# Kernel tuning notes

Measured on AMD Instinct MI355X. Metric: run time of the kernel, lower is better.

## Reference

```python
import jax, jax.numpy as jnp
import numpy as np

NEG_INF = -1e9  # matches the torch module's masked_fill value of -1000000000.0


def setup_inputs() -> dict:
    key = jax.random.key(0)
    kq, kk, kv, km = jax.random.split(key, 4)
    b, h, L, d = 2, 16, 2048, 64
    q = jax.random.normal(kq, (b, h, L, d), dtype=jnp.float32)
    k = jax.random.normal(kk, (b, h, L, d), dtype=jnp.float32)
    v = jax.random.normal(kv, (b, h, L, d), dtype=jnp.float32)
    attn_mask = jax.random.randint(km, (b, 1, L, L), 0, 2, dtype=jnp.int32)
    return {"q": q, "k": k, "v": v, "attn_mask": attn_mask}


def reference(q, k, v, attn_mask):
    # att = q @ k^T / sqrt(d)   -> [b, h, Lq, Lk]
    scale = 1.0 / jnp.sqrt(jnp.asarray(q.shape[-1], q.dtype))
    att = jnp.einsum("bhqd,bhkd->bhqk", q, k) * scale
    # masked positions (mask == 0) filled with -1e9 before softmax
    att = jnp.where(attn_mask == 0, jnp.asarray(NEG_INF, att.dtype), att)
    att = jax.nn.softmax(att, axis=-1)
    # x = att @ v -> [b, h, Lq, d]
    return jnp.einsum("bhqk,bhkd->bhqd", att, v)
```

## Files before the change

kernel.cpp:

```cpp
#include <hip/hip_runtime.h>


typedef unsigned int u32;
typedef unsigned short u16;
typedef unsigned long long u64;

#define BH 32
#define Lseq 2048
#define Dh 64
#define BM 64

typedef __attribute__((ext_vector_type(8))) short frag_ab;
typedef __attribute__((ext_vector_type(4))) float frag_cd;

__device__ __forceinline__ u16 f2bf(float f) {
    u32 u = __float_as_uint(f);
    u32 r = u + 0x7FFFu + ((u >> 16) & 1u);
    return (u16)(r >> 16);
}

__global__ __launch_bounds__(256) void prep(
    const float* __restrict__ k, const float* __restrict__ v,
    const int* __restrict__ mask,
    u16* __restrict__ kb, u16* __restrict__ vtb, u64* __restrict__ bm)
{
    const int blk = blockIdx.x, tid = threadIdx.x;
    if (blk < 512) {
        int t0 = blk * 256 + tid;
        #pragma unroll
        for (int i = 0; i < 8; i++) {
            int idx = t0 + i * 131072;
            float4 f = ((const float4*)k)[idx];
            ushort4 r;
            r.x = f2bf(f.x); r.y = f2bf(f.y); r.z = f2bf(f.z); r.w = f2bf(f.w);
            ((ushort4*)kb)[idx] = r;
        }
    } else if (blk < 1024) {
        __shared__ u16 T[64 * 72];
        for (int j = 0; j < 2; j++) {
            int job = (blk - 512) * 2 + j;
            int bh = job >> 5, kt = job & 31;
            __syncthreads();
            #pragma unroll
            for (int i = 0; i < 4; i++) {
                int idx = tid + 256 * i;
                int key = idx >> 4, ds = idx & 15;
                float4 f = *(const float4*)(v + ((size_t)(bh * Lseq + kt * 64 + key)) * Dh + ds * 4);
                int d0 = ds * 4;
                T[(d0 + 0) * 72 + key] = f2bf(f.x);
                T[(d0 + 1) * 72 + key] = f2bf(f.y);
                T[(d0 + 2) * 72 + key] = f2bf(f.z);
                T[(d0 + 3) * 72 + key] = f2bf(f.w);
            }
            __syncthreads();
            #pragma unroll
            for (int i = 0; i < 4; i++) {
                int idx = tid + 256 * i;
                int d = idx >> 4, ks = idx & 15;
                *(uint2*)(vtb + ((size_t)(bh * Dh + d)) * Lseq + kt * 64 + ks * 4) =
                    *(const uint2*)&T[d * 72 + ks * 4];
            }
        }
    } else {
        int wv = (blk - 1024) * 4 + (tid >> 6);
        int lane = tid & 63;
        for (int i = 0; i < 64; i++) {
            int widx = wv * 64 + i;
            int rowp = widx >> 5, kt = widx & 31;
            int val = mask[(size_t)rowp * Lseq + kt * 64 + lane];
            u64 bal = __ballot(val != 0);
            if (lane == 0) bm[(size_t)kt * 4096 + rowp] = bal;
        }
    }
}

__global__ __launch_bounds__(256, 4)
void attn_mfma(const float* __restrict__ qg, const u16* __restrict__ kb,
               const u16* __restrict__ vtb, const u64* __restrict__ bm,
               float* __restrict__ outg)
{
    const int bh = blockIdx.y, b = bh >> 4;
    const int q0 = blockIdx.x * BM;
    const int tid = threadIdx.x;
    const int wave = tid >> 6, lane = tid & 63;
    const int c = lane & 15, quad = lane >> 4;
    const int row = q0 + 16 * wave + c;

    __shared__ u16 Ks[64 * 72];
    __shared__ u16 Vs[64 * 72];
    __shared__ u16 Ps[4][16 * 72];

    frag_ab qf[2];
    #pragma unroll
    for (int ks = 0; ks < 2; ks++) {
        const float* p = qg + ((size_t)bh * Lseq + row) * Dh + 32 * ks + 8 * quad;
        float4 f0 = *(const float4*)p;
        float4 f1 = *(const float4*)(p + 4);
        union { u32 w[4]; frag_ab f; } uq;
        uq.w[0] = (u32)f2bf(f0.x * 0.125f) | ((u32)f2bf(f0.y * 0.125f) << 16);
        uq.w[1] = (u32)f2bf(f0.z * 0.125f) | ((u32)f2bf(f0.w * 0.125f) << 16);
        uq.w[2] = (u32)f2bf(f1.x * 0.125f) | ((u32)f2bf(f1.y * 0.125f) << 16);
        uq.w[3] = (u32)f2bf(f1.z * 0.125f) | ((u32)f2bf(f1.w * 0.125f) << 16);
        qf[ks] = uq.f;
    }

    frag_cd o_acc[4];
    #pragma unroll
    for (int dt = 0; dt < 4; dt++) o_acc[dt] = (frag_cd){0.f, 0.f, 0.f, 0.f};
    float m_run = -1e30f, l_run = 0.f;

    for (int kt = 0; kt < Lseq / 64; ++kt) {
        __syncthreads();
        {
            const uint4* ksrc = (const uint4*)(kb + ((size_t)bh * Lseq + kt * 64) * Dh);
            #pragma unroll
            for (int i = 0; i < 2; i++) {
                int idx = tid + 256 * i;
                int key = idx >> 3, ds = idx & 7;
                *(uint4*)&Ks[key * 72 + ds * 8] = ksrc[idx];
            }
            #pragma unroll
            for (int i = 0; i < 2; i++) {
                int idx = tid + 256 * i;
                int d = idx >> 3, k8 = idx & 7;
                *(uint4*)&Vs[d * 72 + k8 * 8] =
                    *(const uint4*)(vtb + ((size_t)bh * Dh + d) * Lseq + kt * 64 + k8 * 8);
            }
        }
        const u64 mw = bm[(size_t)kt * 4096 + b * 2048 + row];
        __syncthreads();

        frag_cd s_acc[4];
        #pragma unroll
        for (int t = 0; t < 4; t++) s_acc[t] = (frag_cd){0.f, 0.f, 0.f, 0.f};
        #pragma unroll
        for (int t = 0; t < 4; t++) {
            frag_ab kf0 = *(const frag_ab*)&Ks[(16 * t + c) * 72 + 8 * quad];
            frag_ab kf1 = *(const frag_ab*)&Ks[(16 * t + c) * 72 + 32 + 8 * quad];
            s_acc[t] = __builtin_amdgcn_mfma_f32_16x16x32_bf16(kf0, qf[0], s_acc[t], 0, 0, 0);
            s_acc[t] = __builtin_amdgcn_mfma_f32_16x16x32_bf16(kf1, qf[1], s_acc[t], 0, 0, 0);
        }

        float mx = s_acc[0][0];
        #pragma unroll
        for (int t = 0; t < 4; t++)
            #pragma unroll
            for (int r = 0; r < 4; r++) mx = fmaxf(mx, s_acc[t][r]);
        mx = fmaxf(mx, __shfl_xor(mx, 16));
        mx = fmaxf(mx, __shfl_xor(mx, 32));
        const float mnew = fmaxf(m_run, mx);
        const float alpha = __expf(m_run - mnew);
        m_run = mnew;

        float lsum = 0.f;
        #pragma unroll
        for (int t = 0; t < 4; t++) {
            u32 mbits = (u32)(mw >> (16 * t + 4 * quad)) & 0xFu;
            #pragma unroll
            for (int r = 0; r < 4; r++) {
                float pv = __expf(s_acc[t][r] - mnew);
                pv = ((mbits >> r) & 1u) ? pv : 0.f;
                s_acc[t][r] = pv;
                lsum += pv;
            }
        }
        l_run = l_run * alpha + lsum;
        #pragma unroll
        for (int dt = 0; dt < 4; dt++) o_acc[dt] *= alpha;

        #pragma unroll
        for (int t = 0; t < 4; t++) {
            u32 p0 = __builtin_amdgcn_perm(__float_as_uint(s_acc[t][1]),
                                           __float_as_uint(s_acc[t][0]), 0x07060302u);
            u32 p1 = __builtin_amdgcn_perm(__float_as_uint(s_acc[t][3]),
                                           __float_as_uint(s_acc[t][2]), 0x07060302u);
            *(uint2*)&Ps[wave][c * 72 + 16 * t + 4 * quad] = make_uint2(p0, p1);
        }
        frag_ab pf0 = *(const frag_ab*)&Ps[wave][c * 72 + 8 * quad];
        frag_ab pf1 = *(const frag_ab*)&Ps[wave][c * 72 + 32 + 8 * quad];

        #pragma unroll
        for (int dt = 0; dt < 4; dt++) {
            frag_ab vf0 = *(const frag_ab*)&Vs[(16 * dt + c) * 72 + 8 * quad];
            frag_ab vf1 = *(const frag_ab*)&Vs[(16 * dt + c) * 72 + 32 + 8 * quad];
            o_acc[dt] = __builtin_amdgcn_mfma_f32_16x16x32_bf16(vf0, pf0, o_acc[dt], 0, 0, 0);
            o_acc[dt] = __builtin_amdgcn_mfma_f32_16x16x32_bf16(vf1, pf1, o_acc[dt], 0, 0, 0);
        }
    }

    float l = l_run;
    l += __shfl_xor(l, 16);
    l += __shfl_xor(l, 32);
    const float inv = 1.0f / l;
    float* orow = outg + ((size_t)bh * Lseq + row) * Dh;
    #pragma unroll
    for (int dt = 0; dt < 4; dt++) {
        *(float4*)(orow + 16 * dt + 4 * quad) =
            make_float4(o_acc[dt][0] * inv, o_acc[dt][1] * inv,
                        o_acc[dt][2] * inv, o_acc[dt][3] * inv);
    }
}

extern "C" void kernel_launch(void* const* d_in, const int* in_sizes, int n_in,
                              void* d_out, int out_size, void* d_ws, size_t ws_size,
                              hipStream_t stream) {
    const float* q    = (const float*)d_in[0];
    const float* k    = (const float*)d_in[1];
    const float* v    = (const float*)d_in[2];
    const int*   mask = (const int*)d_in[3];
    float* out = (float*)d_out;

    char* ws = (char*)d_ws;
    u16* kb  = (u16*)(ws);
    u16* vtb = (u16*)(ws + 8388608);
    u64* bmp = (u64*)(ws + 16777216);

    hipLaunchKernelGGL(prep, dim3(1536), dim3(256), 0, stream, k, v, mask, kb, vtb, bmp);
    hipLaunchKernelGGL(attn_mfma, dim3(Lseq / BM, BH), dim3(256), 0, stream,
                       q, kb, vtb, bmp, out);
}
```

Before: 208.9 us.

## Double-buffer K/V tiles, process two query groups per wave, use exp2 with folded scale

The attention kernel now handles 128 query rows per block, two 16-row groups per wave, so each K/V fragment read from shared memory feeds twice as many MFMAs. K/V tiles are double-buffered, with the next tile prefetched into registers during compute. The softmax scale times log2(e) is folded into the bf16 K conversion so exp2f can replace __expf. The O rescale is skipped when no row max changes, and the prep kernel is split into finer-grained blocks. Higher register use lowers occupancy, and there are half as many blocks.

```diff
diff --git a/kernel.cpp b/kernel.cpp
--- a/kernel.cpp
+++ b/kernel.cpp
@@ -8,7 +8,7 @@
 #define BH 32
 #define Lseq 2048
 #define Dh 64
-#define BM 64
+#define QK_SCALE 0.180336879f
 
 typedef __attribute__((ext_vector_type(8))) short frag_ab;
 typedef __attribute__((ext_vector_type(4))) float frag_cd;
@@ -25,47 +25,45 @@
     u16* __restrict__ kb, u16* __restrict__ vtb, u64* __restrict__ bm)
 {
     const int blk = blockIdx.x, tid = threadIdx.x;
-    if (blk < 512) {
-        int t0 = blk * 256 + tid;
-        #pragma unroll
-        for (int i = 0; i < 8; i++) {
-            int idx = t0 + i * 131072;
+    if (blk < 1024) {
+        #pragma unroll
+        for (int i = 0; i < 4; i++) {
+            int idx = blk * 1024 + i * 256 + tid;
             float4 f = ((const float4*)k)[idx];
             ushort4 r;
-            r.x = f2bf(f.x); r.y = f2bf(f.y); r.z = f2bf(f.z); r.w = f2bf(f.w);
+            r.x = f2bf(f.x * QK_SCALE); r.y = f2bf(f.y * QK_SCALE);
+            r.z = f2bf(f.z * QK_SCALE); r.w = f2bf(f.w * QK_SCALE);
             ((ushort4*)kb)[idx] = r;
         }
-    } else if (blk < 1024) {
+    } else if (blk < 2048) {
         __shared__ u16 T[64 * 72];
-        for (int j = 0; j < 2; j++) {
-            int job = (blk - 512) * 2 + j;
-            int bh = job >> 5, kt = job & 31;
-            __syncthreads();
-            #pragma unroll
-            for (int i = 0; i < 4; i++) {
-                int idx = tid + 256 * i;
-                int key = idx >> 4, ds = idx & 15;
-                float4 f = *(const float4*)(v + ((size_t)(bh * Lseq + kt * 64 + key)) * Dh + ds * 4);
-                int d0 = ds * 4;
-                T[(d0 + 0) * 72 + key] = f2bf(f.x);
-                T[(d0 + 1) * 72 + key] = f2bf(f.y);
-                T[(d0 + 2) * 72 + key] = f2bf(f.z);
-                T[(d0 + 3) * 72 + key] = f2bf(f.w);
-            }
-            __syncthreads();
-            #pragma unroll
-            for (int i = 0; i < 4; i++) {
-                int idx = tid + 256 * i;
-                int d = idx >> 4, ks = idx & 15;
-                *(uint2*)(vtb + ((size_t)(bh * Dh + d)) * Lseq + kt * 64 + ks * 4) =
-                    *(const uint2*)&T[d * 72 + ks * 4];
-            }
+        int job = blk - 1024;
+        int bh = job >> 5, kt = job & 31;
+        #pragma unroll
+        for (int i = 0; i < 4; i++) {
+            int idx = tid + 256 * i;
+            int key = idx >> 4, ds = idx & 15;
+            float4 f = *(const float4*)(v + ((size_t)(bh * Lseq + kt * 64 + key)) * Dh + ds * 4);
+            int d0 = ds * 4;
+            T[(d0 + 0) * 72 + key] = f2bf(f.x);
+            T[(d0 + 1) * 72 + key] = f2bf(f.y);
+            T[(d0 + 2) * 72 + key] = f2bf(f.z);
+            T[(d0 + 3) * 72 + key] = f2bf(f.w);
+        }
+        __syncthreads();
+        #pragma unroll
+        for (int i = 0; i < 4; i++) {
+            int idx = tid + 256 * i;
+            int d = idx >> 4, ks = idx & 15;
+            *(uint2*)(vtb + ((size_t)(bh * Dh + d)) * Lseq + kt * 64 + ks * 4) =
+                *(const uint2*)&T[d * 72 + ks * 4];
         }
     } else {
-        int wv = (blk - 1024) * 4 + (tid >> 6);
+        int wv = (blk - 2048) * 4 + (tid >> 6);
         int lane = tid & 63;
-        for (int i = 0; i < 64; i++) {
-            int widx = wv * 64 + i;
+        #pragma unroll
+        for (int i = 0; i < 16; i++) {
+            int widx = wv * 16 + i;
             int rowp = widx >> 5, kt = widx & 31;
             int val = mask[(size_t)rowp * Lseq + kt * 64 + lane];
             u64 bal = __ballot(val != 0);
@@ -74,130 +72,176 @@
     }
 }
 
-__global__ __launch_bounds__(256, 4)
+__global__ __launch_bounds__(256, 2)
 void attn_mfma(const float* __restrict__ qg, const u16* __restrict__ kb,
                const u16* __restrict__ vtb, const u64* __restrict__ bm,
                float* __restrict__ outg)
 {
     const int bh = blockIdx.y, b = bh >> 4;
-    const int q0 = blockIdx.x * BM;
+    const int q0 = blockIdx.x * 128;
     const int tid = threadIdx.x;
     const int wave = tid >> 6, lane = tid & 63;
     const int c = lane & 15, quad = lane >> 4;
-    const int row = q0 + 16 * wave + c;
-
-    __shared__ u16 Ks[64 * 72];
-    __shared__ u16 Vs[64 * 72];
-    __shared__ u16 Ps[4][16 * 72];
-
-    frag_ab qf[2];
+
+    __shared__ u16 Ks[2][64 * 72];
+    __shared__ u16 Vs[2][64 * 72];
+    __shared__ u16 Ps[4][2][16 * 72];
+
+    frag_ab qf[2][2];
     #pragma unroll
-    for (int ks = 0; ks < 2; ks++) {
-        const float* p = qg + ((size_t)bh * Lseq + row) * Dh + 32 * ks + 8 * quad;
-        float4 f0 = *(const float4*)p;
-        float4 f1 = *(const float4*)(p + 4);
-        union { u32 w[4]; frag_ab f; } uq;
-        uq.w[0] = (u32)f2bf(f0.x * 0.125f) | ((u32)f2bf(f0.y * 0.125f) << 16);
-        uq.w[1] = (u32)f2bf(f0.z * 0.125f) | ((u32)f2bf(f0.w * 0.125f) << 16);
-        uq.w[2] = (u32)f2bf(f1.x * 0.125f) | ((u32)f2bf(f1.y * 0.125f) << 16);
-        uq.w[3] = (u32)f2bf(f1.z * 0.125f) | ((u32)f2bf(f1.w * 0.125f) << 16);
-        qf[ks] = uq.f;
-    }
-
-    frag_cd o_acc[4];
+    for (int g = 0; g < 2; g++)
+        #pragma unroll
+        for (int ks = 0; ks < 2; ks++) {
+            const float* p = qg + ((size_t)bh * Lseq + q0 + 32 * wave + 16 * g + c) * Dh
+                                + 32 * ks + 8 * quad;
+            float4 f0 = *(const float4*)p;
+            float4 f1 = *(const float4*)(p + 4);
+            union { u32 w[4]; frag_ab f; } uq;
+            uq.w[0] = (u32)f2bf(f0.x) | ((u32)f2bf(f0.y) << 16);
+            uq.w[1] = (u32)f2bf(f0.z) | ((u32)f2bf(f0.w) << 16);
+            uq.w[2] = (u32)f2bf(f1.x) | ((u32)f2bf(f1.y) << 16);
+            uq.w[3] = (u32)f2bf(f1.z) | ((u32)f2bf(f1.w) << 16);
+            qf[g][ks] = uq.f;
+        }
+
+    frag_cd o_acc[4][2];
     #pragma unroll
-    for (int dt = 0; dt < 4; dt++) o_acc[dt] = (frag_cd){0.f, 0.f, 0.f, 0.f};
-    float m_run = -1e30f, l_run = 0.f;
-
-    for (int kt = 0; kt < Lseq / 64; ++kt) {
-        __syncthreads();
-        {
-            const uint4* ksrc = (const uint4*)(kb + ((size_t)bh * Lseq + kt * 64) * Dh);
+    for (int dt = 0; dt < 4; dt++)
+        #pragma unroll
+        for (int g = 0; g < 2; g++) o_acc[dt][g] = (frag_cd){0.f, 0.f, 0.f, 0.f};
+    float m_run[2] = {-1e30f, -1e30f};
+    float l_run[2] = {0.f, 0.f};
+
+    {
+        const uint4* ksrc = (const uint4*)(kb + ((size_t)bh * Lseq) * Dh);
+        #pragma unroll
+        for (int i = 0; i < 2; i++) {
+            int idx = tid + 256 * i;
+            *(uint4*)&Ks[0][(idx >> 3) * 72 + (idx & 7) * 8] = ksrc[idx];
+            *(uint4*)&Vs[0][(idx >> 3) * 72 + (idx & 7) * 8] =
+                *(const uint4*)(vtb + ((size_t)(bh * Dh + (idx >> 3))) * Lseq + (idx & 7) * 8);
+        }
+    }
+    __syncthreads();
+
+    for (int kt = 0; kt < 32; ++kt) {
+        const int cur = kt & 1, nxt = cur ^ 1;
+        const bool has_next = (kt + 1) < 32;
+
+        u64 mw[2];
+        #pragma unroll
+        for (int g = 0; g < 2; g++)
+            mw[g] = bm[(size_t)kt * 4096 + b * 2048 + q0 + 32 * wave + 16 * g + c];
+
+        uint4 kr[2], vr[2];
+        if (has_next) {
+            const uint4* ksrc = (const uint4*)(kb + ((size_t)bh * Lseq + (kt + 1) * 64) * Dh);
             #pragma unroll
             for (int i = 0; i < 2; i++) {
                 int idx = tid + 256 * i;
-                int key = idx >> 3, ds = idx & 7;
-                *(uint4*)&Ks[key * 72 + ds * 8] = ksrc[idx];
-            }
+                kr[i] = ksrc[idx];
+                vr[i] = *(const uint4*)(vtb + ((size_t)(bh * Dh + (idx >> 3))) * Lseq
+                                        + (kt + 1) * 64 + (idx & 7) * 8);
+            }
+        }
+
+        frag_cd s_acc[2][4];
+        #pragma unroll
+        for (int g = 0; g < 2; g++)
+            #pragma unroll
+            for (int t = 0; t < 4; t++) s_acc[g][t] = (frag_cd){0.f, 0.f, 0.f, 0.f};
+        #pragma unroll
+        for (int t = 0; t < 4; t++) {
+            frag_ab kf0 = *(const frag_ab*)&Ks[cur][(16 * t + c) * 72 + 8 * quad];
+            frag_ab kf1 = *(const frag_ab*)&Ks[cur][(16 * t + c) * 72 + 32 + 8 * quad];
+            #pragma unroll
+            for (int g = 0; g < 2; g++) {
+                s_acc[g][t] = __builtin_amdgcn_mfma_f32_16x16x32_bf16(kf0, qf[g][0], s_acc[g][t], 0, 0, 0);
+                s_acc[g][t] = __builtin_amdgcn_mfma_f32_16x16x32_bf16(kf1, qf[g][1], s_acc[g][t], 0, 0, 0);
+            }
+        }
+
+        frag_ab pf[2][2];
+        #pragma unroll
+        for (int g = 0; g < 2; g++) {
+            float mx = s_acc[g][0][0];
+            #pragma unroll
+            for (int t = 0; t < 4; t++)
+                #pragma unroll
+                for (int r = 0; r < 4; r++) mx = fmaxf(mx, s_acc[g][t][r]);
+            mx = fmaxf(mx, __shfl_xor(mx, 16));
+            mx = fmaxf(mx, __shfl_xor(mx, 32));
+            const float mold = m_run[g];
+            const float mnew = fmaxf(mold, mx);
+            m_run[g] = mnew;
+
+            float lsum = 0.f;
+            #pragma unroll
+            for (int t = 0; t < 4; t++) {
+                u32 mbits = (u32)(mw[g] >> (16 * t + 4 * quad)) & 0xFu;
+                #pragma unroll
+                for (int r = 0; r < 4; r++) {
+                    float pv = exp2f(s_acc[g][t][r] - mnew);
+                    pv = ((mbits >> r) & 1u) ? pv : 0.f;
+                    s_acc[g][t][r] = pv;
+                    lsum += pv;
+                }
+            }
+            if (__any(mnew > mold)) {
+                const float alpha = exp2f(mold - mnew);
+                l_run[g] = l_run[g] * alpha + lsum;
+                #pragma unroll
+                for (int dt = 0; dt < 4; dt++) o_acc[dt][g] *= alpha;
+            } else {
+                l_run[g] += lsum;
+            }
+
+            #pragma unroll
+            for (int t = 0; t < 4; t++) {
+                u32 p0 = __builtin_amdgcn_perm(__float_as_uint(s_acc[g][t][1]),
+                                               __float_as_uint(s_acc[g][t][0]), 0x07060302u);
+                u32 p1 = __builtin_amdgcn_perm(__float_as_uint(s_acc[g][t][3]),
+                                               __float_as_uint(s_acc[g][t][2]), 0x07060302u);
+                *(uint2*)&Ps[wave][g][c * 72 + 16 * t + 4 * quad] = make_uint2(p0, p1);
+            }
+            pf[g][0] = *(const frag_ab*)&Ps[wave][g][c * 72 + 8 * quad];
+            pf[g][1] = *(const frag_ab*)&Ps[wave][g][c * 72 + 32 + 8 * quad];
+        }
+
+        #pragma unroll
+        for (int dt = 0; dt < 4; dt++) {
+            frag_ab vf0 = *(const frag_ab*)&Vs[cur][(16 * dt + c) * 72 + 8 * quad];
+            frag_ab vf1 = *(const frag_ab*)&Vs[cur][(16 * dt + c) * 72 + 32 + 8 * quad];
+            #pragma unroll
+            for (int g = 0; g < 2; g++) {
+                o_acc[dt][g] = __builtin_amdgcn_mfma_f32_16x16x32_bf16(vf0, pf[g][0], o_acc[dt][g], 0, 0, 0);
+                o_acc[dt][g] = __builtin_amdgcn_mfma_f32_16x16x32_bf16(vf1, pf[g][1], o_acc[dt][g], 0, 0, 0);
+            }
+        }
+
+        if (has_next) {
             #pragma unroll
             for (int i = 0; i < 2; i++) {
                 int idx = tid + 256 * i;
-                int d = idx >> 3, k8 = idx & 7;
-                *(uint4*)&Vs[d * 72 + k8 * 8] =
-                    *(const uint4*)(vtb + ((size_t)bh * Dh + d) * Lseq + kt * 64 + k8 * 8);
-            }
-        }
-        const u64 mw = bm[(size_t)kt * 4096 + b * 2048 + row];
+                *(uint4*)&Ks[nxt][(idx >> 3) * 72 + (idx & 7) * 8] = kr[i];
+                *(uint4*)&Vs[nxt][(idx >> 3) * 72 + (idx & 7) * 8] = vr[i];
+            }
+        }
         __syncthreads();
-
-        frag_cd s_acc[4];
-        #pragma unroll
-        for (int t = 0; t < 4; t++) s_acc[t] = (frag_cd){0.f, 0.f, 0.f, 0.f};
-        #pragma unroll
-        for (int t = 0; t < 4; t++) {
-            frag_ab kf0 = *(const frag_ab*)&Ks[(16 * t + c) * 72 + 8 * quad];
-            frag_ab kf1 = *(const frag_ab*)&Ks[(16 * t + c) * 72 + 32 + 8 * quad];
-            s_acc[t] = __builtin_amdgcn_mfma_f32_16x16x32_bf16(kf0, qf[0], s_acc[t], 0, 0, 0);
-            s_acc[t] = __builtin_amdgcn_mfma_f32_16x16x32_bf16(kf1, qf[1], s_acc[t], 0, 0, 0);
-        }
-
-        float mx = s_acc[0][0];
-        #pragma unroll
-        for (int t = 0; t < 4; t++)
-            #pragma unroll
-            for (int r = 0; r < 4; r++) mx = fmaxf(mx, s_acc[t][r]);
-        mx = fmaxf(mx, __shfl_xor(mx, 16));
-        mx = fmaxf(mx, __shfl_xor(mx, 32));
-        const float mnew = fmaxf(m_run, mx);
-        const float alpha = __expf(m_run - mnew);
-        m_run = mnew;
-
-        float lsum = 0.f;
-        #pragma unroll
-        for (int t = 0; t < 4; t++) {
-            u32 mbits = (u32)(mw >> (16 * t + 4 * quad)) & 0xFu;
-            #pragma unroll
-            for (int r = 0; r < 4; r++) {
-                float pv = __expf(s_acc[t][r] - mnew);
-                pv = ((mbits >> r) & 1u) ? pv : 0.f;
-                s_acc[t][r] = pv;
-                lsum += pv;
-            }
-        }
-        l_run = l_run * alpha + lsum;
-        #pragma unroll
-        for (int dt = 0; dt < 4; dt++) o_acc[dt] *= alpha;
-
-        #pragma unroll
-        for (int t = 0; t < 4; t++) {
-            u32 p0 = __builtin_amdgcn_perm(__float_as_uint(s_acc[t][1]),
-                                           __float_as_uint(s_acc[t][0]), 0x07060302u);
-            u32 p1 = __builtin_amdgcn_perm(__float_as_uint(s_acc[t][3]),
-                                           __float_as_uint(s_acc[t][2]), 0x07060302u);
-            *(uint2*)&Ps[wave][c * 72 + 16 * t + 4 * quad] = make_uint2(p0, p1);
-        }
-        frag_ab pf0 = *(const frag_ab*)&Ps[wave][c * 72 + 8 * quad];
-        frag_ab pf1 = *(const frag_ab*)&Ps[wave][c * 72 + 32 + 8 * quad];
-
-        #pragma unroll
-        for (int dt = 0; dt < 4; dt++) {
-            frag_ab vf0 = *(const frag_ab*)&Vs[(16 * dt + c) * 72 + 8 * quad];
-            frag_ab vf1 = *(const frag_ab*)&Vs[(16 * dt + c) * 72 + 32 + 8 * quad];
-            o_acc[dt] = __builtin_amdgcn_mfma_f32_16x16x32_bf16(vf0, pf0, o_acc[dt], 0, 0, 0);
-            o_acc[dt] = __builtin_amdgcn_mfma_f32_16x16x32_bf16(vf1, pf1, o_acc[dt], 0, 0, 0);
-        }
-    }
-
-    float l = l_run;
-    l += __shfl_xor(l, 16);
-    l += __shfl_xor(l, 32);
-    const float inv = 1.0f / l;
-    float* orow = outg + ((size_t)bh * Lseq + row) * Dh;
+    }
+
     #pragma unroll
-    for (int dt = 0; dt < 4; dt++) {
-        *(float4*)(orow + 16 * dt + 4 * quad) =
-            make_float4(o_acc[dt][0] * inv, o_acc[dt][1] * inv,
-                        o_acc[dt][2] * inv, o_acc[dt][3] * inv);
+    for (int g = 0; g < 2; g++) {
+        float l = l_run[g];
+        l += __shfl_xor(l, 16);
+        l += __shfl_xor(l, 32);
+        const float inv = 1.0f / l;
+        float* orow = outg + ((size_t)bh * Lseq + q0 + 32 * wave + 16 * g + c) * Dh;
+        #pragma unroll
+        for (int dt = 0; dt < 4; dt++)
+            *(float4*)(orow + 16 * dt + 4 * quad) =
+                make_float4(o_acc[dt][g][0] * inv, o_acc[dt][g][1] * inv,
+                            o_acc[dt][g][2] * inv, o_acc[dt][g][3] * inv);
     }
 }
 
@@ -215,7 +259,7 @@
     u16* vtb = (u16*)(ws + 8388608);
     u64* bmp = (u64*)(ws + 16777216);
 
-    hipLaunchKernelGGL(prep, dim3(1536), dim3(256), 0, stream, k, v, mask, kb, vtb, bmp);
-    hipLaunchKernelGGL(attn_mfma, dim3(Lseq / BM, BH), dim3(256), 0, stream,
+    hipLaunchKernelGGL(prep, dim3(4096), dim3(256), 0, stream, k, v, mask, kb, vtb, bmp);
+    hipLaunchKernelGGL(attn_mfma, dim3(Lseq / 128, BH), dim3(256), 0, stream,
                        q, kb, vtb, bmp, out);
 }
```

New measurement: 200.9 us. 1.04x faster.
